# Kernel tuning notes

Measured on AMD Instinct MI355X. Metric: run time of the kernel, lower is better.

The kernel has to match this reference:

```python
import jax, jax.numpy as jnp
import numpy as np

B, S, D = 1, 2048, 128   # batch, seq_len, num_hidden (== head dim)
H, KVH = 32, 8           # num_heads, num_kv_heads
REP = H // KVH           # num_rep = 4
D_K = 128                # softmax scale denominator sqrt(d_k)
ROPE_THETA = 10000.0


def _rope(x):
    # x: (B, h, S, D). Standard rotate-half RoPE over last dim, positions on axis -2.
    inv_freq = 1.0 / (ROPE_THETA ** (jnp.arange(0, D, 2, dtype=jnp.float32) / D))  # (D/2,)
    ang = jnp.arange(S, dtype=jnp.float32)[:, None] * inv_freq                      # (S, D/2)
    cos = jnp.concatenate([jnp.cos(ang), jnp.cos(ang)], axis=-1)                    # (S, D)
    sin = jnp.concatenate([jnp.sin(ang), jnp.sin(ang)], axis=-1)
    x1, x2 = jnp.split(x, 2, axis=-1)
    rot = jnp.concatenate([-x2, x1], axis=-1)
    return x * cos + rot * sin


def setup_inputs() -> dict:
    key = jax.random.key(0)
    ks = jax.random.split(key, 11)
    w = 0.02
    return {
        "query":  jax.random.normal(ks[0], (B, S, D), jnp.float32),
        "keys":   jax.random.normal(ks[1], (B, S, D), jnp.float32),
        "values": jax.random.normal(ks[2], (B, S, D), jnp.float32),
        "Wq": jax.random.normal(ks[3], (D, H * D), jnp.float32) * w,
        "bq": jnp.zeros((H * D,), jnp.float32),
        "Wk": jax.random.normal(ks[4], (D, KVH * D), jnp.float32) * w,
        "bk": jnp.zeros((KVH * D,), jnp.float32),
        "Wv": jax.random.normal(ks[5], (D, KVH * D), jnp.float32) * w,
        "bv": jnp.zeros((KVH * D,), jnp.float32),
        "Wo": jax.random.normal(ks[6], (H * D, D), jnp.float32) * w,
        "bo": jnp.zeros((D,), jnp.float32),
    }


def reference(query, keys, values, Wq, bq, Wk, bk, Wv, bv, Wo, bo):
    # Projections; faithful to torch .view(): plain reshape (B,S,h*D)->(B,h,S,D), no transpose.
    q = (query @ Wq + bq).reshape(B, H, S, D)
    k = (keys @ Wk + bk).reshape(B, KVH, S, D)
    v = (values @ Wv + bv).reshape(B, KVH, S, D)
    k = _rope(k)
    v = _rope(v)  # module applies RoPE to values too
    # torch repeat tiles kv heads: q head i <-> kv head (i % KVH).
    qg = q.reshape(B, REP, KVH, S, D)
    scores = jnp.einsum('brgsd,bgtd->brgst', qg, k) / jnp.sqrt(jnp.float32(D_K))
    attn = jax.nn.softmax(scores, axis=-1)  # mask=False path, no causal mask
    out = jnp.einsum('brgst,bgtd->brgsd', attn, v).reshape(B, H, S, D)
    out = out.transpose(0, 2, 1, 3).reshape(B, S, H * D)
    return out @ Wo + bo
```

## Files before the change

kernel.cpp:

```cpp
#include <hip/hip_runtime.h>
#include <math.h>


#define SCALE 0.08838834764831843f
#define L2_10K_64 0.20762050593045952f

typedef short bf16x8 __attribute__((ext_vector_type(8)));
typedef float f32x4 __attribute__((ext_vector_type(4)));

__device__ __forceinline__ unsigned short f2b(float f) {
  union { float f; unsigned u; } x; x.f = f;
  return (unsigned short)((x.u + 0x7FFFu + ((x.u >> 16) & 1u)) >> 16);
}
__device__ __forceinline__ float b2f(unsigned short b) {
  union { unsigned u; float f; } x; x.u = ((unsigned)b) << 16;
  return x.f;
}
__device__ __forceinline__ void lds_dma16(void* lds, const void* g) {
  __builtin_amdgcn_global_load_lds(
      (const __attribute__((address_space(1))) unsigned int*)g,
      (__attribute__((address_space(3))) unsigned int*)lds, 16, 0, 0);
}
__device__ __forceinline__ bf16x8 ldx8(const float* p) {
  f32x4 x0 = *(const f32x4*)p;
  f32x4 x1 = *(const f32x4*)(p + 4);
  bf16x8 a;
#pragma unroll
  for (int j = 0; j < 4; ++j) a[j] = (short)f2b(x0[j]);
#pragma unroll
  for (int j = 0; j < 4; ++j) a[4 + j] = (short)f2b(x1[j]);
  return a;
}

__global__ __launch_bounds__(256) void prep_weights(
    const float* __restrict__ Wk, const float* __restrict__ Wv,
    const float* __restrict__ Wo, const float* __restrict__ Wq,
    const float* __restrict__ bo,
    unsigned short* __restrict__ Wkt, unsigned short* __restrict__ Wvt,
    unsigned short* __restrict__ Wot, unsigned short* __restrict__ Wq2,
    float* __restrict__ out, int big) {
  __shared__ unsigned short T[64][66];
  int b = blockIdx.x, tid = threadIdx.x;
  const float* W;
  unsigned short* D;
  int K, N, tk, tn;
  if (b < 32) {
    W = Wk; D = Wkt; K = 128; N = 1024; int ti = b;       tk = ti & 1;  tn = ti >> 1;
  } else if (b < 64) {
    W = Wv; D = Wvt; K = 128; N = 1024; int ti = b - 32;  tk = ti & 1;  tn = ti >> 1;
  } else if (b < 192) {
    W = Wo; D = Wot; K = 4096; N = 128; int ti = b - 64;  tk = ti >> 1; tn = ti & 1;
  } else if (b < 320) {
    if (!big) {
      int i0 = ((b - 192) * 256 + tid) * 16;
#pragma unroll
      for (int j = 0; j < 16; ++j) Wq2[i0 + j] = f2b(Wq[i0 + j]);
      return;
    }
    W = Wq; D = Wq2; K = 128; N = 4096; int ti = b - 192; tk = ti & 1;  tn = ti >> 1;
  } else {
    int i0 = ((b - 320) * 256 + tid) * 16;
#pragma unroll
    for (int j = 0; j < 16; ++j) out[i0 + j] = bo[(i0 + j) & 127];
    return;
  }
  int k0 = tk * 64, n0 = tn * 64;
  int c = tid & 63, q = tid >> 6;
#pragma unroll
  for (int i = 0; i < 16; ++i) {
    int r = i * 4 + q;
    T[r][c] = f2b(W[(size_t)(k0 + r) * N + n0 + c]);
  }
  __syncthreads();
#pragma unroll
  for (int i = 0; i < 16; ++i) {
    int r = i * 4 + q;
    D[(size_t)(n0 + r) * K + k0 + c] = T[c][r];
  }
}

__global__ __launch_bounds__(256) void proj_all(
    const float* __restrict__ keys, const float* __restrict__ values,
    const float* __restrict__ query,
    const unsigned short* __restrict__ Wkt, const unsigned short* __restrict__ Wvt,
    const unsigned short* __restrict__ Wqt,
    const float* __restrict__ bk, const float* __restrict__ bv, const float* __restrict__ bq,
    unsigned short* __restrict__ kp, unsigned short* __restrict__ vt,
    unsigned short* __restrict__ qp) {
  int bx = blockIdx.x, m0 = blockIdx.y * 64;
  int tid = threadIdx.x;
  int w = tid >> 6, l = tid & 63;
  int l16 = l & 15, g4 = l >> 4;
  int arow = m0 + w * 16 + l16;
  const f32x4 fz = {0.f, 0.f, 0.f, 0.f};

  if (bx >= 16) {
    int n0 = (bx - 16) * 256;
    f32x4 acc[16];
#pragma unroll
    for (int nb = 0; nb < 16; ++nb) acc[nb] = fz;
#pragma unroll
    for (int kc = 0; kc < 4; ++kc) {
      int kbase = kc * 32 + g4 * 8;
      bf16x8 a = ldx8(query + (size_t)arow * 128 + kbase);
#pragma unroll
      for (int nb = 0; nb < 16; ++nb) {
        bf16x8 b = *(const bf16x8*)(Wqt + (size_t)(n0 + nb * 16 + l16) * 128 + kbase);
        acc[nb] = __builtin_amdgcn_mfma_f32_16x16x32_bf16(a, b, acc[nb], 0, 0, 0);
      }
    }
#pragma unroll
    for (int nb = 0; nb < 16; ++nb) {
      int n = n0 + nb * 16 + l16;
      float bvv = bq[n];
#pragma unroll
      for (int r = 0; r < 4; ++r) {
        int mi = m0 + w * 16 + g4 * 4 + r;
        int h = mi >> 6;
        int s = ((mi & 63) << 5) | (n >> 7);
        qp[((size_t)h * 2048 + s) * 128 + (n & 127)] = f2b(acc[nb][r] + bvv);
      }
    }
    return;
  }

  int vmode = bx >> 3;
  int n0 = (bx & 7) * 128, tb = bx & 7;
  const float* X = vmode ? values : keys;
  const unsigned short* Wt = vmode ? Wvt : Wkt;
  const float* bias = vmode ? bv : bk;
  f32x4 acc[8];
#pragma unroll
  for (int nb = 0; nb < 8; ++nb) acc[nb] = fz;
#pragma unroll
  for (int kc = 0; kc < 4; ++kc) {
    int kbase = kc * 32 + g4 * 8;
    bf16x8 a = ldx8(X + (size_t)arow * 128 + kbase);
#pragma unroll
    for (int nb = 0; nb < 8; ++nb) {
      bf16x8 b = *(const bf16x8*)(Wt + (size_t)(n0 + nb * 16 + l16) * 128 + kbase);
      acc[nb] = __builtin_amdgcn_mfma_f32_16x16x32_bf16(a, b, acc[nb], 0, 0, 0);
    }
  }
#pragma unroll
  for (int nb = 0; nb < 4; ++nb) {
    int d2 = nb * 16 + l16;
    float invf = exp2f(-(float)d2 * L2_10K_64);
    float blo = bias[n0 + d2], bhi = bias[n0 + d2 + 64];
#pragma unroll
    for (int r = 0; r < 4; ++r) {
      int mi = m0 + w * 16 + g4 * 4 + r;
      int t = (mi & 255) * 8 + tb;
      float ang = (float)t * invf;
      float sf, cf;
      __sincosf(ang, &sf, &cf);
      float x1 = acc[nb][r] + blo;
      float x2 = acc[nb + 4][r] + bhi;
      unsigned short lo = f2b(x1 * cf - x2 * sf);
      unsigned short hi = f2b(x2 * cf + x1 * sf);
      int g = mi >> 8;
      if (vmode) {
        vt[(size_t)g * 262144 + (size_t)d2 * 2048 + t] = lo;
        vt[(size_t)g * 262144 + (size_t)(d2 + 64) * 2048 + t] = hi;
      } else {
        kp[(size_t)g * 262144 + (size_t)t * 128 + d2] = lo;
        kp[(size_t)g * 262144 + (size_t)t * 128 + d2 + 64] = hi;
      }
    }
  }
}

__global__ void ws_marker(float* __restrict__ out) {
  out[blockIdx.x * 256 + threadIdx.x] = 12345.0f;
}

template <int FUSED_Q>
__global__ __launch_bounds__(256, 2) void attn_kernel(
    const float* __restrict__ X, const unsigned short* __restrict__ Wqb,
    const float* __restrict__ bq, const unsigned short* __restrict__ qp,
    const unsigned short* __restrict__ kp, const unsigned short* __restrict__ vt,
    const unsigned short* __restrict__ Wot, float* __restrict__ out) {
  __shared__ __align__(16) char smem[43008];
  int bid = blockIdx.x;
  int h = bid & 31, g = h & 7;
  int qi0 = (bid >> 5) * 128;
  int tid = threadIdx.x;
  int w = tid >> 6, l = tid & 63;
  int l16 = l & 15, g4 = l >> 4;

  const f32x4 fz = {0.f, 0.f, 0.f, 0.f};
  bf16x8 qfrag[2][4];

  if (FUSED_Q) {
    unsigned short* Uni = (unsigned short*)smem;
    int r0 = h * 64 + (qi0 >> 5);
    int col0 = tid * 16;
#pragma unroll
    for (int jp = 0; jp < 2; ++jp) {
      float acc[2][16];
#pragma unroll
      for (int j = 0; j < 2; ++j)
#pragma unroll
        for (int cc = 0; cc < 16; ++cc) acc[j][cc] = bq[col0 + cc];
      const float* xr0 = X + (size_t)(r0 + jp * 2) * 128;
      const float* xr1 = xr0 + 128;
      for (int k = 0; k < 128; ++k) {
        float x0 = xr0[k], x1 = xr1[k];
        bf16x8 w0 = *(const bf16x8*)(Wqb + (size_t)k * 4096 + col0);
        bf16x8 w1 = *(const bf16x8*)(Wqb + (size_t)k * 4096 + col0 + 8);
#pragma unroll
        for (int e = 0; e < 8; ++e) {
          float f0 = b2f((unsigned short)w0[e]), f1 = b2f((unsigned short)w1[e]);
          acc[0][e] += x0 * f0; acc[0][8 + e] += x0 * f1;
          acc[1][e] += x1 * f0; acc[1][8 + e] += x1 * f1;
        }
      }
#pragma unroll
      for (int j = 0; j < 2; ++j)
#pragma unroll
        for (int cc = 0; cc < 16; ++cc)
          Uni[(jp * 2 + j) * 4096 + col0 + cc] = f2b(acc[j][cc]);
    }
    __syncthreads();
#pragma unroll
    for (int a = 0; a < 2; ++a) {
      int srow = w * 32 + a * 16 + l16;
      int sj = srow >> 5, scol = (srow & 31) * 128;
#pragma unroll
      for (int kc = 0; kc < 4; ++kc)
        qfrag[a][kc] = *(const bf16x8*)&Uni[sj * 4096 + scol + kc * 32 + g4 * 8];
    }
    __syncthreads();
  } else {
#pragma unroll
    for (int a = 0; a < 2; ++a) {
      const unsigned short* qrow =
          qp + ((size_t)h * 2048 + qi0 + w * 32 + a * 16 + l16) * 128;
#pragma unroll
      for (int kc = 0; kc < 4; ++kc)
        qfrag[a][kc] = *(const bf16x8*)(qrow + kc * 32 + g4 * 8);
    }
  }

  const char* kg = (const char*)(kp + (size_t)g * 262144);
  const char* vg = (const char*)(vt + (size_t)g * 262144);
  unsigned short* PsW = (unsigned short*)(smem + 32768) + w * 1280;

#define STAGE_K(tn, kb)                                                          \
  {                                                                              \
    _Pragma("unroll") for (int i = 0; i < 2; ++i) {                              \
      int off = w * 2048 + i * 1024 + l * 16;                                    \
      int row = off >> 8, ch = (off >> 4) & 15;                                  \
      int rch = ch ^ (row & 7);                                                  \
      lds_dma16(smem + (kb) * 8192 + w * 2048 + i * 1024,                        \
                kg + (size_t)(tn) * 8192 + (size_t)row * 256 + rch * 16);        \
    }                                                                            \
  }
#define STAGE_V(tn, vb)                                                          \
  {                                                                              \
    _Pragma("unroll") for (int i = 0; i < 2; ++i) {                              \
      int off = w * 2048 + i * 1024 + l * 16;                                    \
      int vrow = off >> 6, vcb = off & 63;                                       \
      lds_dma16(smem + 16384 + (vb) * 8192 + w * 2048 + i * 1024,                \
                vg + (size_t)vrow * 4096 + (size_t)(tn) * 64 + vcb);             \
    }                                                                            \
  }

  STAGE_K(0, 0);
  STAGE_V(0, 0);
  __syncthreads();

  f32x4 oacc[2][8];
#pragma unroll
  for (int a = 0; a < 2; ++a)
#pragma unroll
    for (int db = 0; db < 8; ++db) oacc[a][db] = fz;
  float lacc[2][4] = {{0.f, 0.f, 0.f, 0.f}, {0.f, 0.f, 0.f, 0.f}};

  int c = 0;
  for (int t = 0; t < 64; ++t) {
    if (t < 63) {
      STAGE_K(t + 1, c ^ 1);
      STAGE_V(t + 1, c ^ 1);
    }

    f32x4 sacc[2][2];
    sacc[0][0] = fz; sacc[0][1] = fz; sacc[1][0] = fz; sacc[1][1] = fz;
    __builtin_amdgcn_s_setprio(1);
#pragma unroll
    for (int kc = 0; kc < 4; ++kc) {
#pragma unroll
      for (int jb = 0; jb < 2; ++jb) {
        int krow = jb * 16 + l16;
        int rch = (kc * 4 + g4) ^ (krow & 7);
        bf16x8 bfrag = *(const bf16x8*)(smem + c * 8192 + krow * 256 + rch * 16);
        sacc[0][jb] = __builtin_amdgcn_mfma_f32_16x16x32_bf16(qfrag[0][kc], bfrag, sacc[0][jb], 0, 0, 0);
        sacc[1][jb] = __builtin_amdgcn_mfma_f32_16x16x32_bf16(qfrag[1][kc], bfrag, sacc[1][jb], 0, 0, 0);
      }
    }
    __builtin_amdgcn_s_setprio(0);
#pragma unroll
    for (int a = 0; a < 2; ++a) {
#pragma unroll
      for (int r = 0; r < 4; ++r) {
        unsigned short u0 = f2b(__expf(sacc[a][0][r] * SCALE));
        unsigned short u1 = f2b(__expf(sacc[a][1][r] * SCALE));
        lacc[a][r] += b2f(u0) + b2f(u1);
        PsW[(a * 16 + g4 * 4 + r) * 40 + l16] = u0;
        PsW[(a * 16 + g4 * 4 + r) * 40 + 16 + l16] = u1;
      }
    }
    bf16x8 pfrag0 = *(const bf16x8*)(PsW + (l16)*40 + g4 * 8);
    bf16x8 pfrag1 = *(const bf16x8*)(PsW + (16 + l16) * 40 + g4 * 8);
    __builtin_amdgcn_s_setprio(1);
#pragma unroll
    for (int db = 0; db < 8; ++db) {
      bf16x8 vfrag = *(const bf16x8*)(smem + 16384 + c * 8192 + (db * 16 + l16) * 64 + g4 * 16);
      oacc[0][db] = __builtin_amdgcn_mfma_f32_16x16x32_bf16(pfrag0, vfrag, oacc[0][db], 0, 0, 0);
      oacc[1][db] = __builtin_amdgcn_mfma_f32_16x16x32_bf16(pfrag1, vfrag, oacc[1][db], 0, 0, 0);
    }
    __builtin_amdgcn_s_setprio(0);
    __syncthreads();
    c ^= 1;
  }

  float invl[2][4];
#pragma unroll
  for (int a = 0; a < 2; ++a)
#pragma unroll
    for (int r = 0; r < 4; ++r) {
      float v = lacc[a][r];
#pragma unroll
      for (int off = 1; off < 16; off <<= 1) v += __shfl_xor(v, off, 64);
      invl[a][r] = 1.f / v;
    }

  unsigned short* Otile = (unsigned short*)smem;
#pragma unroll
  for (int a = 0; a < 2; ++a)
#pragma unroll
    for (int db = 0; db < 8; ++db)
#pragma unroll
      for (int r = 0; r < 4; ++r)
        Otile[(w * 32 + a * 16 + g4 * 4 + r) * 136 + db * 16 + l16] =
            f2b(oacc[a][db][r] * invl[a][r]);
  __syncthreads();
  bf16x8 a2[2][4];
#pragma unroll
  for (int a = 0; a < 2; ++a)
#pragma unroll
    for (int kc = 0; kc < 4; ++kc)
      a2[a][kc] = *(const bf16x8*)&Otile[(w * 32 + a * 16 + l16) * 136 + kc * 32 + g4 * 8];
  f32x4 acc2[2][8];
#pragma unroll
  for (int a = 0; a < 2; ++a)
#pragma unroll
    for (int nb = 0; nb < 8; ++nb) acc2[a][nb] = fz;
#pragma unroll
  for (int kc = 0; kc < 4; ++kc) {
#pragma unroll
    for (int nb = 0; nb < 8; ++nb) {
      bf16x8 b2v = *(const bf16x8*)(Wot + (size_t)(nb * 16 + l16) * 4096 + h * 128 + kc * 32 + g4 * 8);
      acc2[0][nb] = __builtin_amdgcn_mfma_f32_16x16x32_bf16(a2[0][kc], b2v, acc2[0][nb], 0, 0, 0);
      acc2[1][nb] = __builtin_amdgcn_mfma_f32_16x16x32_bf16(a2[1][kc], b2v, acc2[1][nb], 0, 0, 0);
    }
  }
#pragma unroll
  for (int a = 0; a < 2; ++a)
#pragma unroll
    for (int nb = 0; nb < 8; ++nb)
#pragma unroll
      for (int r = 0; r < 4; ++r)
        atomicAdd(&out[(size_t)(qi0 + w * 32 + a * 16 + g4 * 4 + r) * 128 + nb * 16 + l16],
                  acc2[a][nb][r]);
#undef STAGE_K
#undef STAGE_V
}

extern "C" void kernel_launch(void* const* d_in, const int* in_sizes, int n_in,
                              void* d_out, int out_size, void* d_ws, size_t ws_size,
                              hipStream_t stream) {
  const float* query  = (const float*)d_in[0];
  const float* keys   = (const float*)d_in[1];
  const float* values = (const float*)d_in[2];
  const float* Wq = (const float*)d_in[3];
  const float* bq = (const float*)d_in[4];
  const float* Wk = (const float*)d_in[5];
  const float* bk = (const float*)d_in[6];
  const float* Wv = (const float*)d_in[7];
  const float* bv = (const float*)d_in[8];
  const float* Wo = (const float*)d_in[9];
  const float* bo = (const float*)d_in[10];
  float* out = (float*)d_out;
  char* ws = (char*)d_ws;
  const size_t MB = 1024 * 1024;
  if (ws_size < 10 * MB + 512 * 1024) {
    ws_marker<<<1024, 256, 0, stream>>>(out);
    return;
  }
  unsigned short* Wq2   = (unsigned short*)(ws);
  unsigned short* Wkt   = (unsigned short*)(ws + 1 * MB);
  unsigned short* Wvt   = (unsigned short*)(ws + 1 * MB + 256 * 1024);
  unsigned short* Wot   = (unsigned short*)(ws + 1 * MB + 512 * 1024);
  unsigned short* kproj = (unsigned short*)(ws + 2 * MB + 512 * 1024);
  unsigned short* vt    = (unsigned short*)(ws + 6 * MB + 512 * 1024);
  unsigned short* qproj = (unsigned short*)(ws + 10 * MB + 512 * 1024);
  int big = ws_size >= 27 * MB;

  prep_weights<<<384, 256, 0, stream>>>(Wk, Wv, Wo, Wq, bo, Wkt, Wvt, Wot, Wq2, out, big);

  if (big) {
    proj_all<<<dim3(32, 32), 256, 0, stream>>>(keys, values, query, Wkt, Wvt, Wq2,
                                               bk, bv, bq, kproj, vt, qproj);
    attn_kernel<0><<<512, 256, 0, stream>>>(query, Wq2, bq, qproj, kproj, vt, Wot, out);
  } else {
    proj_all<<<dim3(16, 32), 256, 0, stream>>>(keys, values, query, Wkt, Wvt, Wq2,
                                               bk, bv, bq, kproj, vt, qproj);
    attn_kernel<1><<<512, 256, 0, stream>>>(query, Wq2, bq, nullptr, kproj, vt, Wot, out);
  }
}
```

Baseline: 165.3 us.

## Always fuse Q projection into attention kernel using MFMA

Drops the separate Q-projection path, which wrote Q to workspace and re-read it in attention. Q is now always computed inside the attention kernel, using bf16 MFMA against a transposed Wq instead of a scalar FMA loop. Only 4 of the 16 A rows carry data, so most MFMA work is padding, and each block recomputes its Q slice from the full Wq. The intent is to cut a global round trip and a large proj_all grid at the cost of redundant per-block weight reads.

```diff
diff --git a/kernel.cpp b/kernel.cpp
--- a/kernel.cpp
+++ b/kernel.cpp
@@ -37,8 +37,8 @@
     const float* __restrict__ Wo, const float* __restrict__ Wq,
     const float* __restrict__ bo,
     unsigned short* __restrict__ Wkt, unsigned short* __restrict__ Wvt,
-    unsigned short* __restrict__ Wot, unsigned short* __restrict__ Wq2,
-    float* __restrict__ out, int big) {
+    unsigned short* __restrict__ Wot, unsigned short* __restrict__ Wqt,
+    float* __restrict__ out) {
   __shared__ unsigned short T[64][66];
   int b = blockIdx.x, tid = threadIdx.x;
   const float* W;
@@ -51,13 +51,7 @@
   } else if (b < 192) {
     W = Wo; D = Wot; K = 4096; N = 128; int ti = b - 64;  tk = ti >> 1; tn = ti & 1;
   } else if (b < 320) {
-    if (!big) {
-      int i0 = ((b - 192) * 256 + tid) * 16;
-#pragma unroll
-      for (int j = 0; j < 16; ++j) Wq2[i0 + j] = f2b(Wq[i0 + j]);
-      return;
-    }
-    W = Wq; D = Wq2; K = 128; N = 4096; int ti = b - 192; tk = ti & 1;  tn = ti >> 1;
+    W = Wq; D = Wqt; K = 128; N = 4096; int ti = b - 192; tk = ti & 1;  tn = ti >> 1;
   } else {
     int i0 = ((b - 320) * 256 + tid) * 16;
 #pragma unroll
@@ -79,51 +73,17 @@
   }
 }
 
-__global__ __launch_bounds__(256) void proj_all(
+__global__ __launch_bounds__(256) void proj_kv(
     const float* __restrict__ keys, const float* __restrict__ values,
-    const float* __restrict__ query,
     const unsigned short* __restrict__ Wkt, const unsigned short* __restrict__ Wvt,
-    const unsigned short* __restrict__ Wqt,
-    const float* __restrict__ bk, const float* __restrict__ bv, const float* __restrict__ bq,
-    unsigned short* __restrict__ kp, unsigned short* __restrict__ vt,
-    unsigned short* __restrict__ qp) {
+    const float* __restrict__ bk, const float* __restrict__ bv,
+    unsigned short* __restrict__ kp, unsigned short* __restrict__ vt) {
   int bx = blockIdx.x, m0 = blockIdx.y * 64;
   int tid = threadIdx.x;
   int w = tid >> 6, l = tid & 63;
   int l16 = l & 15, g4 = l >> 4;
   int arow = m0 + w * 16 + l16;
   const f32x4 fz = {0.f, 0.f, 0.f, 0.f};
-
-  if (bx >= 16) {
-    int n0 = (bx - 16) * 256;
-    f32x4 acc[16];
-#pragma unroll
-    for (int nb = 0; nb < 16; ++nb) acc[nb] = fz;
-#pragma unroll
-    for (int kc = 0; kc < 4; ++kc) {
-      int kbase = kc * 32 + g4 * 8;
-      bf16x8 a = ldx8(query + (size_t)arow * 128 + kbase);
-#pragma unroll
-      for (int nb = 0; nb < 16; ++nb) {
-        bf16x8 b = *(const bf16x8*)(Wqt + (size_t)(n0 + nb * 16 + l16) * 128 + kbase);
-        acc[nb] = __builtin_amdgcn_mfma_f32_16x16x32_bf16(a, b, acc[nb], 0, 0, 0);
-      }
-    }
-#pragma unroll
-    for (int nb = 0; nb < 16; ++nb) {
-      int n = n0 + nb * 16 + l16;
-      float bvv = bq[n];
-#pragma unroll
-      for (int r = 0; r < 4; ++r) {
-        int mi = m0 + w * 16 + g4 * 4 + r;
-        int h = mi >> 6;
-        int s = ((mi & 63) << 5) | (n >> 7);
-        qp[((size_t)h * 2048 + s) * 128 + (n & 127)] = f2b(acc[nb][r] + bvv);
-      }
-    }
-    return;
-  }
-
   int vmode = bx >> 3;
   int n0 = (bx & 7) * 128, tb = bx & 7;
   const float* X = vmode ? values : keys;
@@ -174,10 +134,9 @@
   out[blockIdx.x * 256 + threadIdx.x] = 12345.0f;
 }
 
-template <int FUSED_Q>
 __global__ __launch_bounds__(256, 2) void attn_kernel(
-    const float* __restrict__ X, const unsigned short* __restrict__ Wqb,
-    const float* __restrict__ bq, const unsigned short* __restrict__ qp,
+    const float* __restrict__ X, const unsigned short* __restrict__ Wqt,
+    const float* __restrict__ bq,
     const unsigned short* __restrict__ kp, const unsigned short* __restrict__ vt,
     const unsigned short* __restrict__ Wot, float* __restrict__ out) {
   __shared__ __align__(16) char smem[43008];
@@ -191,35 +150,33 @@
   const f32x4 fz = {0.f, 0.f, 0.f, 0.f};
   bf16x8 qfrag[2][4];
 
-  if (FUSED_Q) {
+  {
     unsigned short* Uni = (unsigned short*)smem;
     int r0 = h * 64 + (qi0 >> 5);
-    int col0 = tid * 16;
-#pragma unroll
-    for (int jp = 0; jp < 2; ++jp) {
-      float acc[2][16];
-#pragma unroll
-      for (int j = 0; j < 2; ++j)
-#pragma unroll
-        for (int cc = 0; cc < 16; ++cc) acc[j][cc] = bq[col0 + cc];
-      const float* xr0 = X + (size_t)(r0 + jp * 2) * 128;
-      const float* xr1 = xr0 + 128;
-      for (int k = 0; k < 128; ++k) {
-        float x0 = xr0[k], x1 = xr1[k];
-        bf16x8 w0 = *(const bf16x8*)(Wqb + (size_t)k * 4096 + col0);
-        bf16x8 w1 = *(const bf16x8*)(Wqb + (size_t)k * 4096 + col0 + 8);
-#pragma unroll
-        for (int e = 0; e < 8; ++e) {
-          float f0 = b2f((unsigned short)w0[e]), f1 = b2f((unsigned short)w1[e]);
-          acc[0][e] += x0 * f0; acc[0][8 + e] += x0 * f1;
-          acc[1][e] += x1 * f0; acc[1][8 + e] += x1 * f1;
-        }
-      }
-#pragma unroll
-      for (int j = 0; j < 2; ++j)
-#pragma unroll
-        for (int cc = 0; cc < 16; ++cc)
-          Uni[(jp * 2 + j) * 4096 + col0 + cc] = f2b(acc[j][cc]);
+    bf16x8 afrag[4];
+#pragma unroll
+    for (int kc = 0; kc < 4; ++kc) {
+      if (l16 < 4)
+        afrag[kc] = ldx8(X + (size_t)(r0 + l16) * 128 + kc * 32 + g4 * 8);
+      else {
+        bf16x8 z = {0, 0, 0, 0, 0, 0, 0, 0};
+        afrag[kc] = z;
+      }
+    }
+    for (int nb = 0; nb < 64; ++nb) {
+      int n0 = w * 1024 + nb * 16;
+      f32x4 acc = fz;
+#pragma unroll
+      for (int kc = 0; kc < 4; ++kc) {
+        bf16x8 b = *(const bf16x8*)(Wqt + (size_t)(n0 + l16) * 128 + kc * 32 + g4 * 8);
+        acc = __builtin_amdgcn_mfma_f32_16x16x32_bf16(afrag[kc], b, acc, 0, 0, 0);
+      }
+      if (g4 == 0) {
+        float bvv = bq[n0 + l16];
+#pragma unroll
+        for (int r = 0; r < 4; ++r)
+          Uni[r * 4096 + n0 + l16] = f2b(acc[r] + bvv);
+      }
     }
     __syncthreads();
 #pragma unroll
@@ -231,15 +188,6 @@
         qfrag[a][kc] = *(const bf16x8*)&Uni[sj * 4096 + scol + kc * 32 + g4 * 8];
     }
     __syncthreads();
-  } else {
-#pragma unroll
-    for (int a = 0; a < 2; ++a) {
-      const unsigned short* qrow =
-          qp + ((size_t)h * 2048 + qi0 + w * 32 + a * 16 + l16) * 128;
-#pragma unroll
-      for (int kc = 0; kc < 4; ++kc)
-        qfrag[a][kc] = *(const bf16x8*)(qrow + kc * 32 + g4 * 8);
-    }
   }
 
   const char* kg = (const char*)(kp + (size_t)g * 262144);
@@ -398,24 +346,14 @@
     ws_marker<<<1024, 256, 0, stream>>>(out);
     return;
   }
-  unsigned short* Wq2   = (unsigned short*)(ws);
+  unsigned short* Wqt   = (unsigned short*)(ws);
   unsigned short* Wkt   = (unsigned short*)(ws + 1 * MB);
   unsigned short* Wvt   = (unsigned short*)(ws + 1 * MB + 256 * 1024);
   unsigned short* Wot   = (unsigned short*)(ws + 1 * MB + 512 * 1024);
   unsigned short* kproj = (unsigned short*)(ws + 2 * MB + 512 * 1024);
   unsigned short* vt    = (unsigned short*)(ws + 6 * MB + 512 * 1024);
-  unsigned short* qproj = (unsigned short*)(ws + 10 * MB + 512 * 1024);
-  int big = ws_size >= 27 * MB;
-
-  prep_weights<<<384, 256, 0, stream>>>(Wk, Wv, Wo, Wq, bo, Wkt, Wvt, Wot, Wq2, out, big);
-
-  if (big) {
-    proj_all<<<dim3(32, 32), 256, 0, stream>>>(keys, values, query, Wkt, Wvt, Wq2,
-                                               bk, bv, bq, kproj, vt, qproj);
-    attn_kernel<0><<<512, 256, 0, stream>>>(query, Wq2, bq, qproj, kproj, vt, Wot, out);
-  } else {
-    proj_all<<<dim3(16, 32), 256, 0, stream>>>(keys, values, query, Wkt, Wvt, Wq2,
-                                               bk, bv, bq, kproj, vt, qproj);
-    attn_kernel<1><<<512, 256, 0, stream>>>(query, Wq2, bq, nullptr, kproj, vt, Wot, out);
-  }
-}
+
+  prep_weights<<<384, 256, 0, stream>>>(Wk, Wv, Wo, Wq, bo, Wkt, Wvt, Wot, Wqt, out);
+  proj_kv<<<dim3(16, 32), 256, 0, stream>>>(keys, values, Wkt, Wvt, bk, bv, kproj, vt);
+  attn_kernel<<<512, 256, 0, stream>>>(query, Wqt, bq, kproj, vt, Wot, out);
+}
```

Measured after the change: 208.7 us. +26.2%, slower.
